# Optimization experiments

Measured on AMD Instinct MI355X. Metric: run time of the kernel, lower is better.

The kernel has to match this reference:

```python
import jax, jax.numpy as jnp
import numpy as np

B, D, H, T, F = 2, 256, 8, 128, 64
C = H * F          # channels = 512
TE = 512           # time_embed_dim


def setup_inputs() -> dict:
    key = jax.random.key(0)
    ks = jax.random.split(key, 9)
    pd = jax.random.randint(ks[2], (B, T, T), 0, 2 * T - 1, dtype=jnp.int32) - (T - 1)
    s = 0.02
    return {
        "qk": jax.random.normal(ks[0], (B, D, H, T, F), jnp.float32),
        "temb": jax.random.normal(ks[1], (B, T, TE), jnp.float32),
        "pairwise_distances": pd,
        "w_dist": jax.random.normal(ks[3], (3, C), jnp.float32) * s,
        "b_dist": jax.random.normal(ks[4], (C,), jnp.float32) * s,
        "w_time": jax.random.normal(ks[5], (TE, C), jnp.float32) * s,
        "b_time": jax.random.normal(ks[6], (C,), jnp.float32) * s,
        "w_out": jax.random.normal(ks[7], (C, C), jnp.float32) * s,
        "b_out": jax.random.normal(ks[8], (C,), jnp.float32) * s,
    }


def _rpe_net(temb, pd, w_dist, b_dist, w_time, b_time, w_out, b_out):
    d = pd.astype(jnp.float32)
    # (B, T, S, 3): log(1+d+), log(1+d-), indicator(d==0)
    dist_embs = jnp.stack(
        [jnp.log1p(jnp.maximum(d, 0.0)),
         jnp.log1p(jnp.maximum(-d, 0.0)),
         (pd == 0).astype(jnp.float32)],
        axis=-1,
    )
    emb = (temb @ w_time + b_time)[:, :, None, :] + dist_embs @ w_dist + b_dist  # (B,T,S,C)
    R = jax.nn.silu(emb) @ w_out + b_out  # (B,T,S,C)
    return R.reshape(*pd.shape, H, F)     # (B,T,S,H,F)


def reference(qk, temb, pairwise_distances, w_dist, b_dist, w_time, b_time, w_out, b_out):
    R = _rpe_net(temb, pairwise_distances, w_dist, b_dist, w_time, b_time, w_out, b_out)
    # forward_qk: contract head_dim f for every (t, s) pair
    return jnp.einsum('bdhtf,btshf->bdhts', qk, R)
```

## Files before the change

### kernel.cpp

```cpp
#include <hip/hip_runtime.h>
#include <hip/hip_bf16.h>

#define B_  2
#define D_  256
#define H_  8
#define T_  128
#define S_  128
#define F_  64
#define C_  512
#define TE_ 512

typedef _Float16 f16x8 __attribute__((ext_vector_type(8)));
typedef _Float16 f16x4 __attribute__((ext_vector_type(4)));
typedef float    f32x4 __attribute__((ext_vector_type(4)));

#define AS1 __attribute__((address_space(1)))
#define AS3 __attribute__((address_space(3)))

__global__ __launch_bounds__(128) void k_time_proj(
    const float* __restrict__ temb, const float* __restrict__ w_time,
    const float* __restrict__ b_time, const float* __restrict__ b_dist,
    float* __restrict__ tp)
{
    int row = blockIdx.x;
    int tid = threadIdx.x;
    __shared__ float te[TE_];
    for (int i = tid; i < TE_; i += 128)
        te[i] = temb[(size_t)row * TE_ + i];
    __syncthreads();
    int c0 = tid * 4;
    float4 b0 = *(const float4*)&b_time[c0];
    float4 b1 = *(const float4*)&b_dist[c0];
    float ax0 = 0.f, ay0 = 0.f, az0 = 0.f, aw0 = 0.f;
    float ax1 = 0.f, ay1 = 0.f, az1 = 0.f, aw1 = 0.f;
#pragma unroll 4
    for (int e = 0; e < TE_; e += 2) {
        float s0 = te[e], s1 = te[e + 1];
        float4 w0 = *(const float4*)&w_time[(size_t)e * C_ + c0];
        float4 w1 = *(const float4*)&w_time[(size_t)(e + 1) * C_ + c0];
        ax0 += s0 * w0.x; ay0 += s0 * w0.y; az0 += s0 * w0.z; aw0 += s0 * w0.w;
        ax1 += s1 * w1.x; ay1 += s1 * w1.y; az1 += s1 * w1.z; aw1 += s1 * w1.w;
    }
    float4 r;
    r.x = b0.x + b1.x + ax0 + ax1;
    r.y = b0.y + b1.y + ay0 + ay1;
    r.z = b0.z + b1.z + az0 + az1;
    r.w = b0.w + b1.w + aw0 + aw1;
    *(float4*)&tp[(size_t)row * C_ + c0] = r;
}

__global__ __launch_bounds__(128) void k_embed_silu(
    const float* __restrict__ tp, const int* __restrict__ pd,
    const float* __restrict__ w_dist, _Float16* __restrict__ A)
{
    int row = blockIdx.x;
    int bt  = row >> 7;
    int d   = pd[row];
    float f0 = log1pf(fmaxf((float)d, 0.f));
    float f1 = log1pf(fmaxf((float)(-d), 0.f));
    float f2 = (d == 0) ? 1.f : 0.f;
    int c0 = threadIdx.x * 4;
    float4 t4 = *(const float4*)&tp[(size_t)bt * C_ + c0];
    float4 w0 = *(const float4*)&w_dist[c0];
    float4 w1 = *(const float4*)&w_dist[C_ + c0];
    float4 w2 = *(const float4*)&w_dist[2 * C_ + c0];
    float e0 = t4.x + f0 * w0.x + f1 * w1.x + f2 * w2.x;
    float e1 = t4.y + f0 * w0.y + f1 * w1.y + f2 * w2.y;
    float e2 = t4.z + f0 * w0.z + f1 * w1.z + f2 * w2.z;
    float e3 = t4.w + f0 * w0.w + f1 * w1.w + f2 * w2.w;
    f16x4 v;
    v[0] = (_Float16)(e0 / (1.f + expf(-e0)));
    v[1] = (_Float16)(e1 / (1.f + expf(-e1)));
    v[2] = (_Float16)(e2 / (1.f + expf(-e2)));
    v[3] = (_Float16)(e3 / (1.f + expf(-e3)));
    *(f16x4*)&A[(size_t)row * C_ + c0] = v;
}

__global__ __launch_bounds__(512) void k_wt(
    const float* __restrict__ w_out, _Float16* __restrict__ Wt)
{
    int n = blockIdx.x;
    int k = threadIdx.x;
    Wt[(size_t)n * C_ + k] = (_Float16)w_out[(size_t)k * C_ + n];
}

__global__ __launch_bounds__(512) void k_fused(
    const float* __restrict__ qk, const _Float16* __restrict__ A,
    const _Float16* __restrict__ Wt, const float* __restrict__ b_out,
    float* __restrict__ out)
{
    __shared__ alignas(16) _Float16 Rs[128][256];
    __shared__ alignas(16) _Float16 As[128][64];
    __shared__ alignas(16) _Float16 Wts[256][64];

    int bt = blockIdx.x >> 1;
    int hg = blockIdx.x & 1;
    int b  = bt >> 7, t = bt & 127;
    int tid  = threadIdx.x;
    int wave = tid >> 6, lane = tid & 63;
    int mrow = lane & 15, kq = (lane >> 4) * 8;
    int grow = lane >> 3, gcol = (lane & 7) * 8;

    int wm1 = (wave & 1) * 64;
    int wn1 = (wave >> 1) * 64;
    const size_t arow0 = (size_t)bt * 128;
    f32x4 acc[4][4] = {};
    for (int k0 = 0; k0 < 512; k0 += 64) {
#pragma unroll
        for (int q = 0; q < 2; ++q) {
            int ch = wave * 2 + q;
            __builtin_amdgcn_global_load_lds(
                (const AS1 void*)(const void*)&A[(arow0 + ch * 8 + grow) * 512 + k0 + gcol],
                (AS3 void*)(void*)&As[ch * 8][0], 16, 0, 0);
        }
#pragma unroll
        for (int q = 0; q < 4; ++q) {
            int ch = wave * 4 + q;
            __builtin_amdgcn_global_load_lds(
                (const AS1 void*)(const void*)&Wt[(size_t)(hg * 256 + ch * 8 + grow) * 512 + k0 + gcol],
                (AS3 void*)(void*)&Wts[ch * 8][0], 16, 0, 0);
        }
        __syncthreads();
#pragma unroll
        for (int ks = 0; ks < 64; ks += 32) {
            f16x8 af[4], wtf[4];
#pragma unroll
            for (int i = 0; i < 4; ++i) af[i]  = *(const f16x8*)&As[wm1 + i * 16 + mrow][ks + kq];
#pragma unroll
            for (int j = 0; j < 4; ++j) wtf[j] = *(const f16x8*)&Wts[wn1 + j * 16 + mrow][ks + kq];
#pragma unroll
            for (int j = 0; j < 4; ++j)
#pragma unroll
                for (int i = 0; i < 4; ++i)
                    acc[j][i] = __builtin_amdgcn_mfma_f32_16x16x32_f16(wtf[j], af[i], acc[j][i], 0, 0, 0);
        }
        __syncthreads();
    }
    char* rsb = (char*)&Rs[0][0];
    {
        int cg = (lane >> 4) * 4;
#pragma unroll
        for (int j = 0; j < 4; ++j) {
            int c = wn1 + j * 16 + cg;
            float4 bo = *(const float4*)&b_out[hg * 256 + c];
#pragma unroll
            for (int i = 0; i < 4; ++i) {
                int s = wm1 + i * 16 + mrow;
                f16x4 hv;
                hv[0] = (_Float16)(acc[j][i][0] + bo.x);
                hv[1] = (_Float16)(acc[j][i][1] + bo.y);
                hv[2] = (_Float16)(acc[j][i][2] + bo.z);
                hv[3] = (_Float16)(acc[j][i][3] + bo.w);
                *(f16x4*)(rsb + ((((s << 8) + c) << 1) ^ ((s & 1) << 6))) = hv;
            }
        }
    }
    __syncthreads();

    int wm2 = (wave >> 1) * 64;
    int wn2 = (wave & 1) * 64;
    const size_t qstr = (size_t)(H_ * T_ * F_);
    const size_t ostr = (size_t)(H_ * T_ * S_);
    int dcol = lane & 15, sb = (lane >> 4) * 4;
    for (int hp = 0; hp < 4; ++hp) {
        int h = hg * 4 + hp;
        const size_t qbase = (size_t)b * (D_ * H_ * T_ * F_) + (size_t)h * (T_ * F_)
                           + (size_t)t * F_;
        f32x4 acc2[4][4] = {};
#pragma unroll
        for (int ks = 0; ks < 64; ks += 32) {
            f16x8 rf[4], qf[4];
#pragma unroll
            for (int j = 0; j < 4; ++j) {
                int s = wn2 + j * 16 + mrow;
                rf[j] = *(const f16x8*)(rsb + ((((s << 8) + hp * 64 + ks + kq) << 1) ^ ((s & 1) << 6)));
            }
#pragma unroll
            for (int i = 0; i < 4; ++i) {
                const float* qp = &qk[qbase + (size_t)(wm2 + i * 16 + mrow) * qstr + ks + kq];
                float4 u = *(const float4*)qp;
                float4 v = *(const float4*)(qp + 4);
                f16x8 a;
                a[0] = (_Float16)u.x; a[1] = (_Float16)u.y;
                a[2] = (_Float16)u.z; a[3] = (_Float16)u.w;
                a[4] = (_Float16)v.x; a[5] = (_Float16)v.y;
                a[6] = (_Float16)v.z; a[7] = (_Float16)v.w;
                qf[i] = a;
            }
#pragma unroll
            for (int j = 0; j < 4; ++j)
#pragma unroll
                for (int i = 0; i < 4; ++i)
                    acc2[j][i] = __builtin_amdgcn_mfma_f32_16x16x32_f16(rf[j], qf[i], acc2[j][i], 0, 0, 0);
        }
        const size_t obase = (size_t)b * (D_ * H_ * T_ * S_) + (size_t)h * (T_ * S_)
                           + (size_t)t * S_;
#pragma unroll
        for (int i = 0; i < 4; ++i) {
            size_t orow = obase + (size_t)(wm2 + i * 16 + dcol) * ostr;
#pragma unroll
            for (int j = 0; j < 4; ++j)
                *(f32x4*)&out[orow + wn2 + j * 16 + sb] = acc2[j][i];
        }
    }
}

extern "C" void kernel_launch(void* const* d_in, const int* in_sizes, int n_in,
                              void* d_out, int out_size, void* d_ws, size_t ws_size,
                              hipStream_t stream) {
    (void)in_sizes; (void)n_in; (void)out_size; (void)ws_size;
    const float* qk     = (const float*)d_in[0];
    const float* temb   = (const float*)d_in[1];
    const int*   pd     = (const int*)d_in[2];
    const float* w_dist = (const float*)d_in[3];
    const float* b_dist = (const float*)d_in[4];
    const float* w_time = (const float*)d_in[5];
    const float* b_time = (const float*)d_in[6];
    const float* w_out  = (const float*)d_in[7];
    const float* b_out  = (const float*)d_in[8];
    float* out = (float*)d_out;

    char* ws = (char*)d_ws;
    float*     tp = (float*)ws;
    _Float16*  Wt = (_Float16*)(ws + 512 * 1024);
    _Float16*  A  = (_Float16*)(ws + 1024 * 1024);

    k_time_proj<<<dim3(B_ * T_), dim3(128), 0, stream>>>(temb, w_time, b_time, b_dist, tp);
    k_wt<<<dim3(C_), dim3(C_), 0, stream>>>(w_out, Wt);
    k_embed_silu<<<dim3(B_ * T_ * S_), dim3(128), 0, stream>>>(tp, pd, w_dist, A);
    k_fused<<<dim3(B_ * T_ * 2), dim3(512), 0, stream>>>(qk, A, Wt, b_out, out);
}
```

Measured before the change: 520.3 us.

## Alias GEMM staging buffers with R tile and XOR-swizzle LDS layouts

Overlaps the A/Wt staging buffers with the R tile in one 64 KB shared buffer, cutting LDS per block so more blocks can be resident per CU. Replaces the row-parity swizzle with an XOR of the 16-byte chunk index by the row, applied consistently to async global-to-LDS loads and fragment reads, to reduce bank conflicts. Adds a launch-bounds occupancy hint that may constrain registers and risk spills.

Result: faster. 500.4 us (-3.8%).

```diff
diff --git a/kernel.cpp b/kernel.cpp
--- a/kernel.cpp
+++ b/kernel.cpp
@@ -84,14 +84,15 @@
     Wt[(size_t)n * C_ + k] = (_Float16)w_out[(size_t)k * C_ + n];
 }
 
-__global__ __launch_bounds__(512) void k_fused(
+__global__ __launch_bounds__(512, 4) void k_fused(
     const float* __restrict__ qk, const _Float16* __restrict__ A,
     const _Float16* __restrict__ Wt, const float* __restrict__ b_out,
     float* __restrict__ out)
 {
-    __shared__ alignas(16) _Float16 Rs[128][256];
-    __shared__ alignas(16) _Float16 As[128][64];
-    __shared__ alignas(16) _Float16 Wts[256][64];
+    __shared__ alignas(16) char smem[65536];
+    char* asb = smem;
+    char* wtb = smem + 16384;
+    char* rsb = smem;
 
     int bt = blockIdx.x >> 1;
     int hg = blockIdx.x & 1;
@@ -99,7 +100,9 @@
     int tid  = threadIdx.x;
     int wave = tid >> 6, lane = tid & 63;
     int mrow = lane & 15, kq = (lane >> 4) * 8;
-    int grow = lane >> 3, gcol = (lane & 7) * 8;
+    int swz  = (mrow & 7) << 4;
+    int grow = lane >> 3;
+    int gcol = ((lane & 7) ^ grow) * 8;
 
     int wm1 = (wave & 1) * 64;
     int wn1 = (wave >> 1) * 64;
@@ -111,23 +114,29 @@
             int ch = wave * 2 + q;
             __builtin_amdgcn_global_load_lds(
                 (const AS1 void*)(const void*)&A[(arow0 + ch * 8 + grow) * 512 + k0 + gcol],
-                (AS3 void*)(void*)&As[ch * 8][0], 16, 0, 0);
+                (AS3 void*)(void*)(asb + ch * 1024), 16, 0, 0);
         }
 #pragma unroll
         for (int q = 0; q < 4; ++q) {
             int ch = wave * 4 + q;
             __builtin_amdgcn_global_load_lds(
                 (const AS1 void*)(const void*)&Wt[(size_t)(hg * 256 + ch * 8 + grow) * 512 + k0 + gcol],
-                (AS3 void*)(void*)&Wts[ch * 8][0], 16, 0, 0);
+                (AS3 void*)(void*)(wtb + ch * 1024), 16, 0, 0);
         }
         __syncthreads();
 #pragma unroll
         for (int ks = 0; ks < 64; ks += 32) {
             f16x8 af[4], wtf[4];
 #pragma unroll
-            for (int i = 0; i < 4; ++i) af[i]  = *(const f16x8*)&As[wm1 + i * 16 + mrow][ks + kq];
-#pragma unroll
-            for (int j = 0; j < 4; ++j) wtf[j] = *(const f16x8*)&Wts[wn1 + j * 16 + mrow][ks + kq];
+            for (int i = 0; i < 4; ++i) {
+                int row = wm1 + i * 16 + mrow;
+                af[i] = *(const f16x8*)(asb + (((row << 7) + ((ks + kq) << 1)) ^ swz));
+            }
+#pragma unroll
+            for (int j = 0; j < 4; ++j) {
+                int row = wn1 + j * 16 + mrow;
+                wtf[j] = *(const f16x8*)(wtb + (((row << 7) + ((ks + kq) << 1)) ^ swz));
+            }
 #pragma unroll
             for (int j = 0; j < 4; ++j)
 #pragma unroll
@@ -136,7 +145,6 @@
         }
         __syncthreads();
     }
-    char* rsb = (char*)&Rs[0][0];
     {
         int cg = (lane >> 4) * 4;
 #pragma unroll
@@ -151,7 +159,7 @@
                 hv[1] = (_Float16)(acc[j][i][1] + bo.y);
                 hv[2] = (_Float16)(acc[j][i][2] + bo.z);
                 hv[3] = (_Float16)(acc[j][i][3] + bo.w);
-                *(f16x4*)(rsb + ((((s << 8) + c) << 1) ^ ((s & 1) << 6))) = hv;
+                *(f16x4*)(rsb + (((s << 9) + (c << 1)) ^ swz)) = hv;
             }
         }
     }
@@ -173,7 +181,7 @@
 #pragma unroll
             for (int j = 0; j < 4; ++j) {
                 int s = wn2 + j * 16 + mrow;
-                rf[j] = *(const f16x8*)(rsb + ((((s << 8) + hp * 64 + ks + kq) << 1) ^ ((s & 1) << 6)));
+                rf[j] = *(const f16x8*)(rsb + (((s << 9) + ((hp * 64 + ks + kq) << 1)) ^ swz));
             }
 #pragma unroll
             for (int i = 0; i < 4; ++i) {
```
